# Kernel tuning notes

Hardware: AMD Instinct MI355X
Metric: run time of the kernel (lower is better)

## Reference

```python
import jax, jax.numpy as jnp
import numpy as np

DIM_MODEL = 512
DIM_HEAD = 64


def setup_inputs() -> dict:
    key = jax.random.key(0)
    ks = jax.random.split(key, 7)
    B, S = 4, 4096
    x = jax.random.normal(ks[0], (B, S, DIM_MODEL), dtype=jnp.float32)
    mask = jnp.ones((B, 1, S), dtype=jnp.int32)
    # torch Linear init: U(-1/sqrt(fan_in), 1/sqrt(fan_in)); stored as (in, out) for x @ W
    bound = 1.0 / np.sqrt(DIM_MODEL)
    Wq = jax.random.uniform(ks[1], (DIM_MODEL, DIM_HEAD), minval=-bound, maxval=bound, dtype=jnp.float32)
    bq = jax.random.uniform(ks[2], (DIM_HEAD,), minval=-bound, maxval=bound, dtype=jnp.float32)
    Wk = jax.random.uniform(ks[3], (DIM_MODEL, DIM_HEAD), minval=-bound, maxval=bound, dtype=jnp.float32)
    bk = jax.random.uniform(ks[4], (DIM_HEAD,), minval=-bound, maxval=bound, dtype=jnp.float32)
    Wv = jax.random.uniform(ks[5], (DIM_MODEL, DIM_HEAD), minval=-bound, maxval=bound, dtype=jnp.float32)
    bv = jax.random.uniform(ks[6], (DIM_HEAD,), minval=-bound, maxval=bound, dtype=jnp.float32)
    return {"x": x, "mask": mask, "Wq": Wq, "bq": bq, "Wk": Wk, "bk": bk, "Wv": Wv, "bv": bv}


def reference(x, mask, Wq, bq, Wk, bk, Wv, bv):
    # single-head QKV projection
    q = x @ Wq + bq  # (B, S, Dh)
    k = x @ Wk + bk
    v = x @ Wv + bv
    dot_scale = jnp.sqrt(jnp.float32(DIM_HEAD))
    # explicit O(S^2) score matrix, softmax over keys
    scores = jnp.einsum("bqd,bkd->bqk", q, k) / dot_scale  # (B, S, S)
    attn = jax.nn.softmax(scores, axis=-1)
    # faithful to source: mask applied AFTER softmax with -inf fill
    attn = jnp.where(mask == 0, jnp.float32(-jnp.inf), attn)
    return jnp.einsum("bqk,bkd->bqd", attn, v)  # (B, S, Dh)
```

## Files before the change

kernel.cpp:

```cpp
#include <hip/hip_runtime.h>
#include <hip/hip_bf16.h>

typedef _Float16 half8v __attribute__((ext_vector_type(8)));
typedef _Float16 half4v __attribute__((ext_vector_type(4)));
typedef _Float16 half2v __attribute__((ext_vector_type(2)));
typedef __fp16   fp16x2 __attribute__((ext_vector_type(2)));
typedef __attribute__((ext_vector_type(4))) float floatx4;

#define LOG2E_OVER_8 0.18033688011112042f

#if __has_builtin(__builtin_amdgcn_exp2f)
#define EXP2(x) __builtin_amdgcn_exp2f(x)
#else
#define EXP2(x) exp2f(x)
#endif


__global__ __launch_bounds__(256) void wtrans_k(const float* __restrict__ Wq,
                                                const float* __restrict__ Wk,
                                                const float* __restrict__ Wv,
                                                _Float16* __restrict__ Wt) {
    int idx = blockIdx.x * 256 + threadIdx.x;
    int p = idx >> 15, rem = idx & 32767;
    int k = rem >> 6;
    int n = rem & 63;
    const float* W = (p == 0) ? Wq : ((p == 1) ? Wk : Wv);
    int ctg = p * 4 + (n >> 4), m = n & 15;
    int kc = k >> 5, quad = (k >> 3) & 3, j = k & 7;
    Wt[(((ctg << 4) + kc) * 64 + (quad << 4) + m) * 8 + j] = (_Float16)W[k * 64 + n];
}

#define XS_STRIDE 536
__global__ __launch_bounds__(256) void proj_k(const float* __restrict__ x,
                                              const _Float16* __restrict__ Wt,
                                              const float* __restrict__ bq,
                                              const float* __restrict__ bk,
                                              const float* __restrict__ bv,
                                              _Float16* __restrict__ Qh,
                                              _Float16* __restrict__ Kh,
                                              _Float16* __restrict__ Vh) {
    __shared__ _Float16 xs[2][16 * XS_STRIDE];

    int tid = threadIdx.x, l = tid & 63, wv = tid >> 6;
    int m = l & 15, quad = l >> 4;
    int row0 = blockIdx.x * 32;

#pragma unroll
    for (int s = 0; s < 2; s++)
#pragma unroll
        for (int i = 0; i < 8; i++) {
            int idx = tid + i * 256;
            int row = idx >> 7, c4 = idx & 127;
            float4 v = *(const float4*)(x + (row0 + s * 16 + row) * 512 + c4 * 4);
            union { half2v h[2]; uint2 u; } cv;
            cv.h[0][0] = (_Float16)v.x; cv.h[0][1] = (_Float16)v.y;
            cv.h[1][0] = (_Float16)v.z; cv.h[1][1] = (_Float16)v.w;
            *(uint2*)(xs[s] + row * XS_STRIDE + c4 * 4) = cv.u;
        }
    __syncthreads();

    const _Float16* arow0 = xs[0] + m * XS_STRIDE + quad * 8;
    const _Float16* arow1 = xs[1] + m * XS_STRIDE + quad * 8;

    floatx4 acc[2][3];
#pragma unroll
    for (int s = 0; s < 2; s++)
#pragma unroll
        for (int i = 0; i < 3; i++) acc[s][i] = (floatx4)(0.f);

#pragma unroll 4
    for (int kc = 0; kc < 16; kc++) {
        half8v a0 = *(const half8v*)(arow0 + kc * 32);
        half8v a1 = *(const half8v*)(arow1 + kc * 32);
#pragma unroll
        for (int ct = 0; ct < 3; ct++) {
            int ctg = wv * 3 + ct;
            half8v b = *(const half8v*)(Wt + (((ctg << 4) + kc) * 64 + l) * 8);
            acc[0][ct] = __builtin_amdgcn_mfma_f32_16x16x32_f16(a0, b, acc[0][ct], 0, 0, 0);
            acc[1][ct] = __builtin_amdgcn_mfma_f32_16x16x32_f16(a1, b, acc[1][ct], 0, 0, 0);
        }
    }

#pragma unroll
    for (int s = 0; s < 2; s++) {
        int rowb = row0 + s * 16;
#pragma unroll
        for (int ct = 0; ct < 3; ct++) {
            int ctg = wv * 3 + ct;
            int col = ctg * 16 + m;
            float bias = (ctg < 4) ? bq[col] : ((ctg < 8) ? bk[col - 64] : bv[col - 128]);
            if (ctg < 8) {
                _Float16* dst = (ctg < 4) ? Qh : Kh;
                float scl = (ctg < 4) ? LOG2E_OVER_8 : 1.0f;
                int dd = (ctg & 3) * 16 + m;
                int c = dd >> 5, quadQ = (dd >> 3) & 3, j = dd & 7;
#pragma unroll
                for (int r = 0; r < 4; r++) {
                    int row = rowb + quad * 4 + r;
                    int chunk = ((row >> 4) << 1) + c;
                    dst[(chunk * 64 + quadQ * 16 + (row & 15)) * 8 + j] =
                        (_Float16)((acc[s][ct][r] + bias) * scl);
                }
            } else {
                int dt = ctg - 8;
                int t64 = rowb >> 6, ktp = (rowb >> 5) & 1, half = (rowb >> 4) & 1;
                int chunk = t64 * 8 + dt * 2 + ktp;
                union { _Float16 h[4]; unsigned long long u; } pk;
#pragma unroll
                for (int r = 0; r < 4; r++) pk.h[r] = (_Float16)(acc[s][ct][r] + bias);
                *(unsigned long long*)(Vh + (chunk * 64 + quad * 16 + m) * 8 + half * 4) = pk.u;
            }
        }
    }
}

template <int NT>
__global__ __launch_bounds__(256, 6) void attn_k(const _Float16* __restrict__ Qh,
                                                 const _Float16* __restrict__ Kh,
                                                 const _Float16* __restrict__ Vh,
                                                 const int* __restrict__ mask,
                                                 _Float16* __restrict__ Np,
                                                 float* __restrict__ Dp,
                                                 int gshift) {
    __shared__ float T[4][16 * 68];

    int tid = threadIdx.x, l = tid & 63, wv = tid >> 6;
    int m = l & 15, quad = l >> 4;
    int bid = blockIdx.x;
    int grp = bid & ((1 << gshift) - 1), qblk = bid >> gshift;
    int os = grp >> 2, b = grp & 3;
    int q0 = qblk * 64 + wv * 16;

    const int* maskb = mask + b * 4096 + os * (NT * 64);
    int az = 0;
#pragma unroll
    for (int i = 0; i < NT; i++) az |= (maskb[l + i * 64] == 0);
    const bool hasz = __any(az);

    int qt_g = (b * 4096 + q0) >> 4;
    half8v qf[2];
#pragma unroll
    for (int c = 0; c < 2; c++)
        qf[c] = *(const half8v*)(Qh + ((qt_g * 2 + c) * 64 + l) * 8);

    half8v ones8;
#pragma unroll
    for (int i = 0; i < 8; i++) ones8[i] = (_Float16)1.0f;

    int tb0 = (b * 64 + os * NT) * 512;
    const uint4* kh4 = (const uint4*)Kh + tb0;
    const uint4* vh4 = (const uint4*)Vh + tb0;

    floatx4 oacc[4];
#pragma unroll
    for (int dt = 0; dt < 4; dt++) oacc[dt] = (floatx4)(0.f);
    floatx4 oden = (floatx4)(0.f);

    for (int t = 0; t < NT; t++) {
        const uint4* kt4 = kh4 + t * 512;
        const uint4* vt4 = vh4 + t * 512;
#pragma unroll
        for (int sp = 0; sp < 2; sp++) {
            union { uint4 u; half8v h; } kk[4];
#pragma unroll
            for (int i = 0; i < 4; i++)
                kk[i].u = kt4[(sp * 4 + i) * 64 + l];
            uint4 vv[4];
#pragma unroll
            for (int dt = 0; dt < 4; dt++)
                vv[dt] = vt4[(dt * 2 + sp) * 64 + l];
            half8v pb8;
            {
                union { fp16x2 h2[4]; half8v h8; } pu;
#pragma unroll
                for (int se = 0; se < 2; se++) {
                    floatx4 sf = (floatx4)(0.f);
                    __builtin_amdgcn_s_setprio(1);
                    sf = __builtin_amdgcn_mfma_f32_16x16x32_f16(kk[se * 2 + 0].h, qf[0], sf, 0, 0, 0);
                    sf = __builtin_amdgcn_mfma_f32_16x16x32_f16(kk[se * 2 + 1].h, qf[1], sf, 0, 0, 0);
                    __builtin_amdgcn_s_setprio(0);
                    float p0 = EXP2(sf[0]), p1 = EXP2(sf[1]);
                    float p2 = EXP2(sf[2]), p3 = EXP2(sf[3]);
                    if (hasz) {
                        int kg = t * 64 + (sp * 2 + se) * 16 + quad * 4;
                        if (maskb[kg + 0] == 0) p0 = -__builtin_inff();
                        if (maskb[kg + 1] == 0) p1 = -__builtin_inff();
                        if (maskb[kg + 2] == 0) p2 = -__builtin_inff();
                        if (maskb[kg + 3] == 0) p3 = -__builtin_inff();
                    }
                    pu.h2[se * 2 + 0] = __builtin_amdgcn_cvt_pkrtz(p0, p1);
                    pu.h2[se * 2 + 1] = __builtin_amdgcn_cvt_pkrtz(p2, p3);
                }
                pb8 = pu.h8;
            }
            __builtin_amdgcn_s_setprio(1);
            oden = __builtin_amdgcn_mfma_f32_16x16x32_f16(ones8, pb8, oden, 0, 0, 0);
#pragma unroll
            for (int dt = 0; dt < 4; dt++) {
                union { uint4 u; half8v h; } vc; vc.u = vv[dt];
                oacc[dt] = __builtin_amdgcn_mfma_f32_16x16x32_f16(vc.h, pb8, oacc[dt], 0, 0, 0);
            }
            __builtin_amdgcn_s_setprio(0);
        }
    }

    float* Tw = &T[wv][0];
    int rowb = os * 16384 + b * 4096 + q0;
    if (l < 16) Dp[rowb + l] = oden[0];
#pragma unroll
    for (int dt = 0; dt < 4; dt++)
#pragma unroll
        for (int r = 0; r < 4; r++)
            Tw[m * 68 + dt * 16 + quad * 4 + r] = oacc[dt][r];
    asm volatile("s_waitcnt lgkmcnt(0)" ::: "memory");
    __builtin_amdgcn_sched_barrier(0);
#pragma unroll
    for (int g = 0; g < 4; g++) {
        int idx = g * 64 + l;
        int row = idx >> 4, c4 = (idx & 15) * 4;
        float4 v = *(const float4*)(Tw + row * 68 + c4);
        union { half4v h; unsigned long long u; } pk;
        pk.h[0] = (_Float16)v.x; pk.h[1] = (_Float16)v.y;
        pk.h[2] = (_Float16)v.z; pk.h[3] = (_Float16)v.w;
        *(unsigned long long*)(Np + (size_t)(rowb + row) * 64 + c4) = pk.u;
    }
}

__global__ __launch_bounds__(256) void combine_k(const _Float16* __restrict__ Np,
                                                 const float* __restrict__ Dp,
                                                 float* __restrict__ out,
                                                 int spl) {
    int g4 = blockIdx.x * 256 + threadIdx.x;
    int row = g4 >> 4;
    float4 nu = make_float4(0.f, 0.f, 0.f, 0.f);
    float d = 0.f;
    for (int sp = 0; sp < spl; sp++) {
        union { unsigned long long u; half4v h; } v;
        v.u = *(const unsigned long long*)(Np + ((size_t)sp << 20) + (size_t)g4 * 4);
        nu.x += (float)v.h[0]; nu.y += (float)v.h[1];
        nu.z += (float)v.h[2]; nu.w += (float)v.h[3];
        d += Dp[sp * 16384 + row];
    }
    float inv = 1.0f / d;
    ((float4*)out)[g4] = make_float4(nu.x * inv, nu.y * inv, nu.z * inv, nu.w * inv);
}

extern "C" void kernel_launch(void* const* d_in, const int* in_sizes, int n_in,
                              void* d_out, int out_size, void* d_ws, size_t ws_size,
                              hipStream_t stream) {
    const float* x  = (const float*)d_in[0];
    const int* mask = (const int*)d_in[1];
    const float* Wq = (const float*)d_in[2];
    const float* bq = (const float*)d_in[3];
    const float* Wk = (const float*)d_in[4];
    const float* bk = (const float*)d_in[5];
    const float* Wv = (const float*)d_in[6];
    const float* bv = (const float*)d_in[7];
    float* out = (float*)d_out;

    char* ws = (char*)d_ws;
    _Float16* Wt = (_Float16*)(ws);
    _Float16* Qh = (_Float16*)(ws + 0x40000);
    _Float16* Kh = (_Float16*)(ws + 0x240000);
    _Float16* Vh = (_Float16*)(ws + 0x440000);
    float*    Dp = (float*)(ws + 0x640000);
    _Float16* Np = (_Float16*)(ws + 0x740000);

    wtrans_k<<<384, 256, 0, stream>>>(Wq, Wk, Wv, Wt);
    proj_k<<<512, 256, 0, stream>>>(x, Wt, bq, bk, bv, Qh, Kh, Vh);
    attn_k<8><<<64 * 32, 256, 0, stream>>>(Qh, Kh, Vh, mask, Np, Dp, 5);
    combine_k<<<1024, 256, 0, stream>>>(Np, Dp, out, 8);
}
```

Measured before the change: 140.1 us.

## Software-pipeline attention loop: prefetch next K/V and overlap QK with PV

Restructures the inner attention loop into a fully unrolled software pipeline over half-tiles. The next K and V fragments are loaded and the next QK score MFMAs are issued before the current PV MFMAs, with V double-buffered in two register sets. The aim is to hide global load latency and the exp/convert dependency chain behind matrix work. Occupancy is lowered from 6 to 4 waves per SIMD to make room for the extra registers, and full unrolling over 2*NT grows code size.

After: 136.3 us. 2.7% less time.

```diff
diff --git a/kernel.cpp b/kernel.cpp
--- a/kernel.cpp
+++ b/kernel.cpp
@@ -114,8 +114,25 @@
     }
 }
 
+#define LDV_BLOCK(VARR, HN)                                                    \
+    do {                                                                       \
+        _Pragma("unroll")                                                      \
+        for (int dt = 0; dt < 4; dt++)                                         \
+            VARR[dt] = vh4[((HN) >> 1) * 512 + ((HN) & 1) * 64 + dt * 128 + l];\
+    } while (0)
+
+#define PV_BLOCK(VARR)                                                         \
+    do {                                                                       \
+        _Pragma("unroll")                                                      \
+        for (int dt = 0; dt < 4; dt++) {                                       \
+            union { uint4 u; half8v h; } vc; vc.u = VARR[dt];                  \
+            oacc[dt] = __builtin_amdgcn_mfma_f32_16x16x32_f16(vc.h, pb8,       \
+                                                              oacc[dt], 0, 0, 0);\
+        }                                                                      \
+    } while (0)
+
 template <int NT>
-__global__ __launch_bounds__(256, 6) void attn_k(const _Float16* __restrict__ Qh,
+__global__ __launch_bounds__(256, 4) void attn_k(const _Float16* __restrict__ Qh,
                                                  const _Float16* __restrict__ Kh,
                                                  const _Float16* __restrict__ Vh,
                                                  const int* __restrict__ mask,
@@ -156,52 +173,64 @@
     for (int dt = 0; dt < 4; dt++) oacc[dt] = (floatx4)(0.f);
     floatx4 oden = (floatx4)(0.f);
 
-    for (int t = 0; t < NT; t++) {
-        const uint4* kt4 = kh4 + t * 512;
-        const uint4* vt4 = vh4 + t * 512;
-#pragma unroll
-        for (int sp = 0; sp < 2; sp++) {
-            union { uint4 u; half8v h; } kk[4];
-#pragma unroll
-            for (int i = 0; i < 4; i++)
-                kk[i].u = kt4[(sp * 4 + i) * 64 + l];
-            uint4 vv[4];
-#pragma unroll
-            for (int dt = 0; dt < 4; dt++)
-                vv[dt] = vt4[(dt * 2 + sp) * 64 + l];
-            half8v pb8;
-            {
-                union { fp16x2 h2[4]; half8v h8; } pu;
-#pragma unroll
-                for (int se = 0; se < 2; se++) {
-                    floatx4 sf = (floatx4)(0.f);
-                    __builtin_amdgcn_s_setprio(1);
-                    sf = __builtin_amdgcn_mfma_f32_16x16x32_f16(kk[se * 2 + 0].h, qf[0], sf, 0, 0, 0);
-                    sf = __builtin_amdgcn_mfma_f32_16x16x32_f16(kk[se * 2 + 1].h, qf[1], sf, 0, 0, 0);
-                    __builtin_amdgcn_s_setprio(0);
-                    float p0 = EXP2(sf[0]), p1 = EXP2(sf[1]);
-                    float p2 = EXP2(sf[2]), p3 = EXP2(sf[3]);
-                    if (hasz) {
-                        int kg = t * 64 + (sp * 2 + se) * 16 + quad * 4;
-                        if (maskb[kg + 0] == 0) p0 = -__builtin_inff();
-                        if (maskb[kg + 1] == 0) p1 = -__builtin_inff();
-                        if (maskb[kg + 2] == 0) p2 = -__builtin_inff();
-                        if (maskb[kg + 3] == 0) p3 = -__builtin_inff();
-                    }
-                    pu.h2[se * 2 + 0] = __builtin_amdgcn_cvt_pkrtz(p0, p1);
-                    pu.h2[se * 2 + 1] = __builtin_amdgcn_cvt_pkrtz(p2, p3);
+    uint4 kk[4], vva[4], vvb[4];
+    floatx4 sf[2];
+
+#pragma unroll
+    for (int i = 0; i < 4; i++) kk[i] = kh4[i * 64 + l];
+    LDV_BLOCK(vva, 0);
+#pragma unroll
+    for (int se = 0; se < 2; se++) {
+        union { uint4 u; half8v h; } k0, k1;
+        k0.u = kk[se * 2 + 0]; k1.u = kk[se * 2 + 1];
+        floatx4 s = (floatx4)(0.f);
+        s = __builtin_amdgcn_mfma_f32_16x16x32_f16(k0.h, qf[0], s, 0, 0, 0);
+        s = __builtin_amdgcn_mfma_f32_16x16x32_f16(k1.h, qf[1], s, 0, 0, 0);
+        sf[se] = s;
+    }
+
+#pragma unroll
+    for (int h = 0; h < 2 * NT; h++) {
+        const bool more = (h + 1 < 2 * NT);
+        if (more) {
+#pragma unroll
+            for (int i = 0; i < 4; i++) kk[i] = kh4[(h + 1) * 256 + i * 64 + l];
+            if ((h & 1) == 0) LDV_BLOCK(vvb, h + 1); else LDV_BLOCK(vva, h + 1);
+        }
+        half8v pb8;
+        {
+            union { fp16x2 h2[4]; half8v h8; } pu;
+#pragma unroll
+            for (int se = 0; se < 2; se++) {
+                float p0 = EXP2(sf[se][0]), p1 = EXP2(sf[se][1]);
+                float p2 = EXP2(sf[se][2]), p3 = EXP2(sf[se][3]);
+                if (hasz) {
+                    int kg = h * 32 + se * 16 + quad * 4;
+                    if (maskb[kg + 0] == 0) p0 = -__builtin_inff();
+                    if (maskb[kg + 1] == 0) p1 = -__builtin_inff();
+                    if (maskb[kg + 2] == 0) p2 = -__builtin_inff();
+                    if (maskb[kg + 3] == 0) p3 = -__builtin_inff();
                 }
-                pb8 = pu.h8;
+                pu.h2[se * 2 + 0] = __builtin_amdgcn_cvt_pkrtz(p0, p1);
+                pu.h2[se * 2 + 1] = __builtin_amdgcn_cvt_pkrtz(p2, p3);
             }
-            __builtin_amdgcn_s_setprio(1);
-            oden = __builtin_amdgcn_mfma_f32_16x16x32_f16(ones8, pb8, oden, 0, 0, 0);
-#pragma unroll
-            for (int dt = 0; dt < 4; dt++) {
-                union { uint4 u; half8v h; } vc; vc.u = vv[dt];
-                oacc[dt] = __builtin_amdgcn_mfma_f32_16x16x32_f16(vc.h, pb8, oacc[dt], 0, 0, 0);
+            pb8 = pu.h8;
+        }
+        __builtin_amdgcn_s_setprio(1);
+        if (more) {
+#pragma unroll
+            for (int se = 0; se < 2; se++) {
+                union { uint4 u; half8v h; } k0, k1;
+                k0.u = kk[se * 2 + 0]; k1.u = kk[se * 2 + 1];
+                floatx4 s = (floatx4)(0.f);
+                s = __builtin_amdgcn_mfma_f32_16x16x32_f16(k0.h, qf[0], s, 0, 0, 0);
+                s = __builtin_amdgcn_mfma_f32_16x16x32_f16(k1.h, qf[1], s, 0, 0, 0);
+                sf[se] = s;
             }
-            __builtin_amdgcn_s_setprio(0);
-        }
+        }
+        oden = __builtin_amdgcn_mfma_f32_16x16x32_f16(ones8, pb8, oden, 0, 0, 0);
+        if ((h & 1) == 0) PV_BLOCK(vva); else PV_BLOCK(vvb);
+        __builtin_amdgcn_s_setprio(0);
     }
 
     float* Tw = &T[wv][0];
```
